# Kernel tuning notes

Hardware: AMD Instinct MI355X
Metric: run time of the kernel (lower is better)

The kernel has to match this reference:

```python
import jax, jax.numpy as jnp
import numpy as np

# Cl(4,1) conformal geometric algebra: 2^5 = 32 blades, metric (+,+,+,+,-)
_METRIC = np.array([1.0, 1.0, 1.0, 1.0, -1.0], dtype=np.float32)

def _cayley(metric):
    n = len(metric); dim = 1 << n
    C = np.zeros((dim, dim, dim), dtype=np.float32)
    for a in range(dim):
        for b in range(dim):
            # sign from reordering basis vectors into canonical order
            s = 0
            t = a >> 1
            while t:
                s += bin(t & b).count('1')
                t >>= 1
            sign = -1.0 if (s & 1) else 1.0
            # metric contribution from repeated basis vectors
            common = a & b
            for i in range(n):
                if (common >> i) & 1:
                    sign *= metric[i]
            C[a, b, a ^ b] = sign
    return jnp.asarray(C)

CAYLEY = _cayley(_METRIC)  # [32,32,32]

def _manifold_normalize(x, eps=1e-12):
    # normalize each multivector to unit Euclidean norm over its 32 components
    return x * jax.lax.rsqrt(jnp.sum(x * x, axis=-1, keepdims=True) + eps)

def _geometric_product(a, b):
    # a, b: [B,N,H,32] -> [B,N,H,32]
    return jnp.einsum('bnhi,bnhj,ijk->bnhk', a, b, CAYLEY)

def setup_inputs() -> dict:
    key = jax.random.key(0)
    k0, k1, k2, k3, k4 = jax.random.split(key, 5)
    B, S, N, D, H = 16, 256, 64, 6, 16
    x = jax.random.normal(k0, (B, S, N, D), dtype=jnp.float32)
    W_in = jax.random.normal(k1, (D, H * 32), dtype=jnp.float32) * (1.0 / np.sqrt(D))
    b_in = jax.random.normal(k2, (H * 32,), dtype=jnp.float32) * 0.01
    W_out = jax.random.normal(k3, (H * 32, D), dtype=jnp.float32) * (1.0 / np.sqrt(H * 32))
    b_out = jax.random.normal(k4, (D,), dtype=jnp.float32) * 0.01
    return {"x": x, "W_in": W_in, "b_in": b_in, "W_out": W_out, "b_out": b_out}

def reference(x, W_in, b_in, W_out, b_out):
    B, S, N, D = x.shape
    H = W_in.shape[1] // 32
    # project all timesteps at once: [B,S,N,H,32]
    x_embs = (x @ W_in + b_in).reshape(B, S, N, H, 32)
    psi0 = jnp.zeros((B, N, H, 32), dtype=x.dtype).at[..., 0].set(1.0)

    def step(psi, xs):
        u_t, x_t = xs  # [B,N,H,32], [B,N,D]
        delta_r = u_t.at[..., 0].add(1.0)
        delta_r = _manifold_normalize(delta_r)
        psi = _geometric_product(delta_r, psi)
        psi = _manifold_normalize(psi)
        pred_delta = psi.reshape(B, N, H * 32) @ W_out + b_out
        return psi, x_t + pred_delta

    _, outs = jax.lax.scan(step, psi0,
                           (jnp.swapaxes(x_embs, 0, 1), jnp.swapaxes(x, 0, 1)))
    return jnp.swapaxes(outs, 0, 1)  # [B,S,N,D]
```

## Files before the change

kernel.cpp:

```cpp
#include <hip/hip_runtime.h>
#include <stdint.h>

typedef __fp16   pkv2 __attribute__((ext_vector_type(2)));
typedef _Float16 h2   __attribute__((ext_vector_type(2)));

__device__ __forceinline__ uint32_t pk(float a, float b) {
    union { pkv2 h; uint32_t u; } u;
    u.h = __builtin_amdgcn_cvt_pkrtz(a, b);
    return u.u;
}
__device__ __forceinline__ uint32_t pkrne(float a, float b) {
    union { _Float16 f[2]; uint32_t u; } u;
    u.f[0] = (_Float16)a; u.f[1] = (_Float16)b;
    return u.u;
}
__device__ __forceinline__ float dot2u(uint32_t w, uint32_t xp, float c) {
    union { uint32_t u; h2 h; } a, b; a.u = w; b.u = xp;
    return __builtin_amdgcn_fdot2(a.h, b.h, c, false);
}
__device__ __forceinline__ void unpk(uint32_t u, float& a, float& b) {
    union { uint32_t u; h2 h; } x; x.u = u;
    a = (float)x.h.x; b = (float)x.h.y;
}

template<int CTRL>
__device__ __forceinline__ float dppAdd(float v) {
    int sh = __builtin_amdgcn_update_dpp(0, __float_as_int(v), CTRL, 0xF, 0xF, true);
    return v + __int_as_float(sh);
}
__device__ __forceinline__ float rowSum16(float v) {
    v = dppAdd<0xB1>(v);
    v = dppAdd<0x4E>(v);
    v = dppAdd<0x124>(v);
    v = dppAdd<0x128>(v);
    return v;
}


__device__ __forceinline__ void gpC(const float* __restrict__ D,
                                    const float* __restrict__ P,
                                    float* __restrict__ O) {
#pragma unroll
    for (int i = 0; i < 4; ++i) {
#pragma unroll
        for (int j = 0; j < 4; ++j) {
            float re = 0.f, im = 0.f;
#pragma unroll
            for (int k = 0; k < 4; ++k) {
                const float dr = D[(i * 4 + k) * 2], di = D[(i * 4 + k) * 2 + 1];
                const float pr = P[(k * 4 + j) * 2], pi = P[(k * 4 + j) * 2 + 1];
                re = fmaf(dr, pr, re); re = fmaf(-di, pi, re);
                im = fmaf(dr, pi, im); im = fmaf(di, pr, im);
            }
            O[(i * 4 + j) * 2] = re; O[(i * 4 + j) * 2 + 1] = im;
        }
    }
}

__device__ __forceinline__ void embedPair(const uint32_t* __restrict__ wf,
                                          float4 xv1, float2 xw1,
                                          float4 xv2, float2 xw2,
                                          float* __restrict__ D1,
                                          float* __restrict__ D2) {
#pragma unroll
    for (int a = 0; a < 32; ++a) {
        uint4 r = *(const uint4*)(wf + a * 4);
        float w0, w1, w2, w3, w4, w5;
        unpk(r.x, w0, w1); unpk(r.y, w2, w3); unpk(r.z, w4, w5);
        const float bias = __uint_as_float(r.w);
        float d1 = bias, d2 = bias;
        d1 = fmaf(xv1.x, w0, d1);  d2 = fmaf(xv2.x, w0, d2);
        d1 = fmaf(xv1.y, w1, d1);  d2 = fmaf(xv2.y, w1, d2);
        d1 = fmaf(xv1.z, w2, d1);  d2 = fmaf(xv2.z, w2, d2);
        d1 = fmaf(xv1.w, w3, d1);  d2 = fmaf(xv2.w, w3, d2);
        d1 = fmaf(xw1.x, w4, d1);  d2 = fmaf(xw2.x, w4, d2);
        d1 = fmaf(xw1.y, w5, d1);  d2 = fmaf(xw2.y, w5, d2);
        D1[a] = d1; D2[a] = d2;
    }
}

__device__ __forceinline__ void nrmF(float* __restrict__ v) {
    float s0 = 0.f, s1 = 0.f, s2 = 0.f, s3 = 0.f;
#pragma unroll
    for (int k = 0; k < 32; k += 4) {
        s0 = fmaf(v[k], v[k], s0);  s1 = fmaf(v[k + 1], v[k + 1], s1);
        s2 = fmaf(v[k + 2], v[k + 2], s2);  s3 = fmaf(v[k + 3], v[k + 3], s3);
    }
    float rs = rsqrtf(fmaf((s0 + s1) + (s2 + s3), 0.25f, 1e-12f));
#pragma unroll
    for (int k = 0; k < 32; ++k) v[k] *= rs;
}

__device__ __forceinline__ void scanC(const float* __restrict__ D,
                                      const uint32_t* __restrict__ ps,
                                      float* __restrict__ R) {
    float p[32];
#pragma unroll
    for (int mq = 0; mq < 4; ++mq) {
        uint4 v = *(const uint4*)(ps + mq * 4);
        unpk(v.x, p[8 * mq + 0], p[8 * mq + 1]);
        unpk(v.y, p[8 * mq + 2], p[8 * mq + 3]);
        unpk(v.z, p[8 * mq + 4], p[8 * mq + 5]);
        unpk(v.w, p[8 * mq + 6], p[8 * mq + 7]);
    }
    gpC(D, p, R);
}

__device__ __forceinline__ void packTQ(const float* __restrict__ v,
                                       uint32_t* __restrict__ dst) {
#pragma unroll
    for (int mq = 0; mq < 4; ++mq)
        *(uint4*)(dst + mq * 4) =
            make_uint4(pk(v[8 * mq + 0], v[8 * mq + 1]), pk(v[8 * mq + 2], v[8 * mq + 3]),
                       pk(v[8 * mq + 4], v[8 * mq + 5]), pk(v[8 * mq + 6], v[8 * mq + 7]));
}

__device__ __forceinline__ float emitOut(const float* __restrict__ P,
                                         const uint32_t* __restrict__ woh,
                                         float4 xv, float2 xw,
                                         const float* __restrict__ bo,
                                         int h, int b, int n, int t,
                                         float* __restrict__ out) {
    float s0 = 0.f, s1 = 0.f, s2 = 0.f, s3 = 0.f;
#pragma unroll
    for (int k = 0; k < 32; k += 4) {
        s0 = fmaf(P[k], P[k], s0);  s1 = fmaf(P[k + 1], P[k + 1], s1);
        s2 = fmaf(P[k + 2], P[k + 2], s2);  s3 = fmaf(P[k + 3], P[k + 3], s3);
    }
    float rs = rsqrtf(fmaf((s0 + s1) + (s2 + s3), 0.25f, 1e-12f));
    uint32_t ph[16];
#pragma unroll
    for (int m = 0; m < 16; ++m) ph[m] = pk(P[2 * m], P[2 * m + 1]);
    float pd[6];
#pragma unroll
    for (int dd = 0; dd < 6; ++dd) {
        uint4 w0 = *(const uint4*)(woh + dd * 16);
        uint4 w1 = *(const uint4*)(woh + dd * 16 + 4);
        uint4 w2 = *(const uint4*)(woh + dd * 16 + 8);
        uint4 w3 = *(const uint4*)(woh + dd * 16 + 12);
        float a0 = dot2u(w0.x, ph[0], 0.f);
        a0 = dot2u(w0.y, ph[1], a0);  a0 = dot2u(w0.z, ph[2], a0);
        a0 = dot2u(w0.w, ph[3], a0);  a0 = dot2u(w1.x, ph[4], a0);
        a0 = dot2u(w1.y, ph[5], a0);  a0 = dot2u(w1.z, ph[6], a0);
        a0 = dot2u(w1.w, ph[7], a0);
        float a1 = dot2u(w2.x, ph[8], 0.f);
        a1 = dot2u(w2.y, ph[9], a1);  a1 = dot2u(w2.z, ph[10], a1);
        a1 = dot2u(w2.w, ph[11], a1); a1 = dot2u(w3.x, ph[12], a1);
        a1 = dot2u(w3.y, ph[13], a1); a1 = dot2u(w3.z, ph[14], a1);
        a1 = dot2u(w3.w, ph[15], a1);
        pd[dd] = rowSum16((a0 + a1) * rs);
    }
    float v = pd[0] + xv.x + bo[0];
    v = (h == 1) ? pd[1] + xv.y + bo[1] : v;
    v = (h == 2) ? pd[2] + xv.z + bo[2] : v;
    v = (h == 3) ? pd[3] + xv.w + bo[3] : v;
    v = (h == 4) ? pd[4] + xw.x + bo[4] : v;
    v = (h == 5) ? pd[5] + xw.y + bo[5] : v;
    if (h < 6)
        out[(((size_t)b * 256 + t) * 64 + n) * 6 + h] = v;
    return rs;
}

#define SXBASE(t) ((t) * 6 + ((t) >> 5) * 4)
#define LOADX2(t, xv1, xw1, xv2, xw2)                               \
    { float4 p0 = *(const float4*)&sX[SXBASE(t)];                   \
      float4 p1 = *(const float4*)&sX[SXBASE(t) + 4];               \
      float4 p2 = *(const float4*)&sX[SXBASE(t) + 8];               \
      xv1 = p0; xw1 = make_float2(p1.x, p1.y);                      \
      xv2 = make_float4(p1.z, p1.w, p2.x, p2.y);                    \
      xw2 = make_float2(p2.z, p2.w); }

__global__ void prep(const float* __restrict__ W_in, const float* __restrict__ b_in,
                     const float* __restrict__ W_out,
                     uint32_t* __restrict__ wsWF, uint32_t* __restrict__ wsWo) {
    __shared__ float Gre[32][16], Gim[32][16];
    const int tid = threadIdx.x;

    if (tid < 32) {
        float gre[5][16] = {{0}}, gim[5][16] = {{0}};
        gre[0][0] = 1;  gre[0][5] = 1;  gre[0][10] = -1; gre[0][15] = -1;
        gre[1][2] = 1;  gre[1][7] = 1;  gre[1][8] = 1;   gre[1][13] = 1;
        gim[2][3] = 1;  gim[2][6] = 1;  gim[2][9] = -1;  gim[2][12] = -1;
        gre[3][3] = 1;  gre[3][6] = -1; gre[3][9] = -1;  gre[3][12] = 1;
        gre[4][2] = 1;  gre[4][7] = -1; gre[4][8] = -1;  gre[4][13] = 1;
        float Mre[16] = {0}, Mim[16] = {0};
        Mre[0] = Mre[5] = Mre[10] = Mre[15] = 1.f;
        for (int g = 0; g < 5; ++g) {
            if (!(tid & (1 << g))) continue;
            float Rre[16], Rim[16];
            for (int i = 0; i < 4; ++i)
                for (int j = 0; j < 4; ++j) {
                    float r = 0.f, s = 0.f;
                    for (int k = 0; k < 4; ++k) {
                        r += Mre[i*4+k]*gre[g][k*4+j] - Mim[i*4+k]*gim[g][k*4+j];
                        s += Mre[i*4+k]*gim[g][k*4+j] + Mim[i*4+k]*gre[g][k*4+j];
                    }
                    Rre[i*4+j] = r; Rim[i*4+j] = s;
                }
            for (int e = 0; e < 16; ++e) { Mre[e] = Rre[e]; Mim[e] = Rim[e]; }
        }
        for (int e = 0; e < 16; ++e) { Gre[tid][e] = Mre[e]; Gim[tid][e] = Mim[e]; }
    }
    __syncthreads();

    for (int e = tid; e < 512; e += blockDim.x) {
        const int h = e >> 5, ent = e & 31;
        const int m = ent >> 1, ri = ent & 1;
        float wv[7];
        for (int d = 0; d < 7; ++d) {
            float acc = 0.f;
            for (int A = 0; A < 32; ++A) {
                const float g = ri ? Gim[A][m] : Gre[A][m];
                const float c = (d < 6) ? W_in[d * 512 + h * 32 + A] : b_in[h * 32 + A];
                acc = fmaf(c, g, acc);
            }
            wv[d] = acc;
        }
        if (ri == 0 && (m == 0 || m == 5 || m == 10 || m == 15))
            wv[6] += 1.f;
        uint32_t* dst = wsWF + e * 4;
        dst[0] = pkrne(wv[0], wv[1]);
        dst[1] = pkrne(wv[2], wv[3]);
        dst[2] = pkrne(wv[4], wv[5]);
        dst[3] = __float_as_uint(wv[6]);
    }

    for (int e = tid; e < 256; e += blockDim.x) {
        const int h = e >> 4, m = e & 15;
        for (int d = 0; d < 6; ++d) {
            float vr = 0.f, vi = 0.f;
            for (int A = 0; A < 32; ++A) {
                const float w = W_out[(h * 32 + A) * 6 + d] * 0.25f;
                vr = fmaf(w, Gre[A][m], vr);
                vi = fmaf(w, Gim[A][m], vi);
            }
            wsWo[h * 96 + d * 16 + m] = pkrne(vr, vi);
        }
    }
}

__global__ __launch_bounds__(128, 1)
void versor(const float* __restrict__ x, const uint32_t* __restrict__ wsWF,
            const float* __restrict__ b_out,
            const uint32_t* __restrict__ wsWo, float* __restrict__ out) {
    __shared__ __align__(16) uint32_t sWF[16 * 132];
    __shared__ __align__(16) float    sX[256 * 6 + 32];
    __shared__ __align__(16) uint32_t sTQ[16 * 164];

    const int tid = threadIdx.x;
    const int bid = blockIdx.x;
    const int chain = (bid & 7) * 128 + (bid >> 3);
    const int b = chain >> 6, n = chain & 63;

    for (int e = tid; e < 512; e += 128) {
        const int h = e >> 5, a = e & 31;
        *(uint4*)&sWF[h * 132 + a * 4] = *(const uint4*)(wsWF + e * 4);
    }
    for (int r = tid; r < 256; r += 128) {
        const float2* s2 = (const float2*)(x + (((size_t)b * 256 + r) * 64 + n) * 6);
        float2 a0 = s2[0], a1 = s2[1], a2 = s2[2];
        float* dst = &sX[SXBASE(r)];
        *(float2*)dst = a0; *(float2*)(dst + 2) = a1; *(float2*)(dst + 4) = a2;
    }

    const int h = tid & 15, c = tid >> 4;
    float bo[6];
#pragma unroll
    for (int dd = 0; dd < 6; ++dd) bo[dd] = b_out[dd];
    __syncthreads();

    const uint32_t* wf  = &sWF[h * 132];
    const uint32_t* woh = wsWo + h * 96;
    uint32_t*       tqh = &sTQ[h * 164];
    const int t0 = c * 32;

    float U[32], O[32], D1[32], D2[32];
    float4 xv1, xv2; float2 xw1, xw2;

    LOADX2(t0, xv1, xw1, xv2, xw2);
    embedPair(wf, xv1, xw1, xv2, xw2, D1, D2);
    gpC(D2, D1, U);
#pragma unroll 1
    for (int q = 1; q < 16; ++q) {
        LOADX2(t0 + 2 * q, xv1, xw1, xv2, xw2);
        embedPair(wf, xv1, xw1, xv2, xw2, D1, D2);
        gpC(D1, U, O);
        gpC(D2, O, U);
        if ((q & 3) == 3) nrmF(U);
    }
    packTQ(U, tqh + c * 20);
    __syncthreads();

#pragma unroll
    for (int j = 0; j < 32; ++j) O[j] = U[j];
#pragma unroll 1
    for (int r = 0; r < 3; ++r) {
        const int s = 1 << r;
        const bool act = (c >= s);
        float R[32];
        if (act) scanC(O, tqh + (c - s) * 20, R);
        __syncthreads();
        if (act) {
            nrmF(R);
#pragma unroll
            for (int j = 0; j < 32; ++j) O[j] = R[j];
            packTQ(O, tqh + c * 20);
        }
        __syncthreads();
    }

    if (c == 0) {
#pragma unroll
        for (int j = 0; j < 32; ++j) U[j] = 0.f;
        U[0] = 1.f; U[10] = 1.f; U[20] = 1.f; U[30] = 1.f;
    } else {
        const uint32_t* ps = tqh + (c - 1) * 20;
#pragma unroll
        for (int mq = 0; mq < 4; ++mq) {
            uint4 v = *(const uint4*)(ps + mq * 4);
            unpk(v.x, U[8 * mq + 0], U[8 * mq + 1]);
            unpk(v.y, U[8 * mq + 2], U[8 * mq + 3]);
            unpk(v.z, U[8 * mq + 4], U[8 * mq + 5]);
            unpk(v.w, U[8 * mq + 6], U[8 * mq + 7]);
        }
    }

#pragma unroll 1
    for (int q = 0; q < 16; ++q) {
        const int t = t0 + 2 * q;
        LOADX2(t, xv1, xw1, xv2, xw2);
        embedPair(wf, xv1, xw1, xv2, xw2, D1, D2);
        gpC(D1, U, O);
        emitOut(O, woh, xv1, xw1, bo, h, b, n, t, out);
        gpC(D2, O, U);
        float rs = emitOut(U, woh, xv2, xw2, bo, h, b, n, t + 1, out);
#pragma unroll
        for (int j = 0; j < 32; ++j) U[j] *= rs;
    }
}

extern "C" void kernel_launch(void* const* d_in, const int* in_sizes, int n_in,
                              void* d_out, int out_size, void* d_ws, size_t ws_size,
                              hipStream_t stream) {
    const float* x     = (const float*)d_in[0];
    const float* W_in  = (const float*)d_in[1];
    const float* b_in  = (const float*)d_in[2];
    const float* W_out = (const float*)d_in[3];
    const float* b_out = (const float*)d_in[4];
    float* out = (float*)d_out;

    uint32_t* wsWF = (uint32_t*)d_ws;
    uint32_t* wsWo = (uint32_t*)((char*)d_ws + 8192);

    prep<<<1, 128, 0, stream>>>(W_in, b_in, W_out, wsWF, wsWo);
    versor<<<1024, 128, 0, stream>>>(x, wsWF, b_out, wsWo, out);
}
```

Baseline: 186.6 us.

## Split each chain's time scan across 16 chunks with 256 threads per block

New measurement: 587.4 us. 215% more time.

```diff
diff --git a/kernel.cpp b/kernel.cpp
--- a/kernel.cpp
+++ b/kernel.cpp
@@ -57,25 +57,19 @@
     }
 }
 
-__device__ __forceinline__ void embedPair(const uint32_t* __restrict__ wf,
-                                          float4 xv1, float2 xw1,
-                                          float4 xv2, float2 xw2,
-                                          float* __restrict__ D1,
-                                          float* __restrict__ D2) {
+__device__ __forceinline__ void embed1(const uint32_t* __restrict__ wf,
+                                       float4 xv, float2 xw,
+                                       float* __restrict__ D) {
 #pragma unroll
     for (int a = 0; a < 32; ++a) {
         uint4 r = *(const uint4*)(wf + a * 4);
         float w0, w1, w2, w3, w4, w5;
         unpk(r.x, w0, w1); unpk(r.y, w2, w3); unpk(r.z, w4, w5);
-        const float bias = __uint_as_float(r.w);
-        float d1 = bias, d2 = bias;
-        d1 = fmaf(xv1.x, w0, d1);  d2 = fmaf(xv2.x, w0, d2);
-        d1 = fmaf(xv1.y, w1, d1);  d2 = fmaf(xv2.y, w1, d2);
-        d1 = fmaf(xv1.z, w2, d1);  d2 = fmaf(xv2.z, w2, d2);
-        d1 = fmaf(xv1.w, w3, d1);  d2 = fmaf(xv2.w, w3, d2);
-        d1 = fmaf(xw1.x, w4, d1);  d2 = fmaf(xw2.x, w4, d2);
-        d1 = fmaf(xw1.y, w5, d1);  d2 = fmaf(xw2.y, w5, d2);
-        D1[a] = d1; D2[a] = d2;
+        float d = __uint_as_float(r.w);
+        d = fmaf(xv.x, w0, d);  d = fmaf(xv.y, w1, d);
+        d = fmaf(xv.z, w2, d);  d = fmaf(xv.w, w3, d);
+        d = fmaf(xw.x, w4, d);  d = fmaf(xw.y, w5, d);
+        D[a] = d;
     }
 }
 
@@ -239,24 +233,26 @@
     }
 }
 
-__global__ __launch_bounds__(128, 1)
+__global__ __launch_bounds__(256)
+__attribute__((amdgpu_num_vgpr(170)))
 void versor(const float* __restrict__ x, const uint32_t* __restrict__ wsWF,
             const float* __restrict__ b_out,
             const uint32_t* __restrict__ wsWo, float* __restrict__ out) {
     __shared__ __align__(16) uint32_t sWF[16 * 132];
     __shared__ __align__(16) float    sX[256 * 6 + 32];
-    __shared__ __align__(16) uint32_t sTQ[16 * 164];
+    __shared__ __align__(16) uint32_t sTQ[16 * 324];
 
     const int tid = threadIdx.x;
     const int bid = blockIdx.x;
     const int chain = (bid & 7) * 128 + (bid >> 3);
     const int b = chain >> 6, n = chain & 63;
 
-    for (int e = tid; e < 512; e += 128) {
+    for (int e = tid; e < 512; e += 256) {
         const int h = e >> 5, a = e & 31;
         *(uint4*)&sWF[h * 132 + a * 4] = *(const uint4*)(wsWF + e * 4);
     }
-    for (int r = tid; r < 256; r += 128) {
+    {
+        const int r = tid;
         const float2* s2 = (const float2*)(x + (((size_t)b * 256 + r) * 64 + n) * 6);
         float2 a0 = s2[0], a1 = s2[1], a2 = s2[2];
         float* dst = &sX[SXBASE(r)];
@@ -271,30 +267,30 @@
 
     const uint32_t* wf  = &sWF[h * 132];
     const uint32_t* woh = wsWo + h * 96;
-    uint32_t*       tqh = &sTQ[h * 164];
-    const int t0 = c * 32;
-
-    float U[32], O[32], D1[32], D2[32];
+    uint32_t*       tqh = &sTQ[h * 324];
+    const int t0 = c * 16;
+
+    float U[32], O[32], D[32];
     float4 xv1, xv2; float2 xw1, xw2;
 
     LOADX2(t0, xv1, xw1, xv2, xw2);
-    embedPair(wf, xv1, xw1, xv2, xw2, D1, D2);
-    gpC(D2, D1, U);
+    embed1(wf, xv1, xw1, U);
+    embed1(wf, xv2, xw2, D);
+    gpC(D, U, O);
 #pragma unroll 1
-    for (int q = 1; q < 16; ++q) {
+    for (int q = 1; q < 8; ++q) {
         LOADX2(t0 + 2 * q, xv1, xw1, xv2, xw2);
-        embedPair(wf, xv1, xw1, xv2, xw2, D1, D2);
-        gpC(D1, U, O);
-        gpC(D2, O, U);
-        if ((q & 3) == 3) nrmF(U);
-    }
-    packTQ(U, tqh + c * 20);
+        embed1(wf, xv1, xw1, D);
+        gpC(D, O, U);
+        embed1(wf, xv2, xw2, D);
+        gpC(D, U, O);
+        if ((q & 3) == 3) nrmF(O);
+    }
+    packTQ(O, tqh + c * 20);
     __syncthreads();
 
-#pragma unroll
-    for (int j = 0; j < 32; ++j) O[j] = U[j];
 #pragma unroll 1
-    for (int r = 0; r < 3; ++r) {
+    for (int r = 0; r < 4; ++r) {
         const int s = 1 << r;
         const bool act = (c >= s);
         float R[32];
@@ -326,13 +322,14 @@
     }
 
 #pragma unroll 1
-    for (int q = 0; q < 16; ++q) {
+    for (int q = 0; q < 8; ++q) {
         const int t = t0 + 2 * q;
         LOADX2(t, xv1, xw1, xv2, xw2);
-        embedPair(wf, xv1, xw1, xv2, xw2, D1, D2);
-        gpC(D1, U, O);
+        embed1(wf, xv1, xw1, D);
+        gpC(D, U, O);
         emitOut(O, woh, xv1, xw1, bo, h, b, n, t, out);
-        gpC(D2, O, U);
+        embed1(wf, xv2, xw2, D);
+        gpC(D, O, U);
         float rs = emitOut(U, woh, xv2, xw2, bo, h, b, n, t + 1, out);
 #pragma unroll
         for (int j = 0; j < 32; ++j) U[j] *= rs;
@@ -353,5 +350,5 @@
     uint32_t* wsWo = (uint32_t*)((char*)d_ws + 8192);
 
     prep<<<1, 128, 0, stream>>>(W_in, b_in, W_out, wsWF, wsWo);
-    versor<<<1024, 128, 0, stream>>>(x, wsWF, b_out, wsWo, out);
-}
+    versor<<<1024, 256, 0, stream>>>(x, wsWF, b_out, wsWo, out);
+}
```
